# Kernel optimization log

Measured on AMD Instinct MI355X. Metric: run time of the kernel, lower is better.

Reference implementation:

```python
import jax, jax.numpy as jnp
import numpy as np

# --- model/problem constants (match init_kwargs) ---
B = 1024      # batch
F = 512       # featureSize
H = 1024      # hiddenSize
S = 8         # symmetrySize
BOX = 12      # boxSize
MAXB = 64     # maxBoxes
MAXSY = 64    # maxSyms
MAXS = 16     # max stack depth (pattern uses <= 2)
L = 126


def setup_inputs() -> dict:
    key = jax.random.key(0)
    ks = jax.random.split(key, 9)

    def lin(k, out_d, in_d):
        k1, k2 = jax.random.split(k)
        bound = 1.0 / np.sqrt(in_d)
        W = jax.random.uniform(k1, (out_d, in_d), minval=-bound, maxval=bound, dtype=jnp.float32)
        b = jax.random.uniform(k2, (out_d,), minval=-bound, maxval=bound, dtype=jnp.float32)
        return W, b

    Wd, bd = lin(ks[0], H, F)      # AdjDecoder.decode
    Wl, bl = lin(ks[1], F, H)      # AdjDecoder.left
    Wr, br = lin(ks[2], F, H)      # AdjDecoder.right
    Wsd, bsd = lin(ks[3], H, F)    # SymDecoder.decode
    Wsf, bsf = lin(ks[4], F, H)    # SymDecoder.left
    Wss, bss = lin(ks[5], S, H)    # SymDecoder.right
    Wbox, bbox = lin(ks[6], BOX, F)  # BoxDecoder.decode

    inputStacks = jax.random.normal(ks[7], (B, F), dtype=jnp.float32)

    # Valid stack program, PROCESSING order: [adj, sym, box] * 42.
    # stack depth: 1 ->(1) 2 ->(2) 2 ->(0) 1 ; 42 boxes, 42 syms.
    proc = np.tile(np.array([1, 2, 0], dtype=np.int32), L // 3)
    stored = proc[::-1].copy()  # forward() processes operations in reverse
    operations = jnp.asarray(np.tile(stored[None, None, :], (B, 1, 1)))  # [B,1,L]

    return {"inputStacks": inputStacks, "operations": operations,
            "Wd": Wd, "bd": bd, "Wl": Wl, "bl": bl, "Wr": Wr, "br": br,
            "Wsd": Wsd, "bsd": bsd, "Wsf": Wsf, "bsf": bsf, "Wss": Wss, "bss": bss,
            "Wbox": Wbox, "bbox": bbox}


def _forward(inputStacks, operations, Wd, bd, Wl, bl, Wr, br,
             Wsd, bsd, Wsf, bsf, Wss, bss, Wbox, bbox):
    Bn, Fn = inputStacks.shape
    ops_proc = jnp.flip(operations[:, 0, :], axis=1).T  # [L, B] processing order

    stack = jnp.zeros((Bn, MAXS, Fn), inputStacks.dtype).at[:, 0, :].set(inputStacks)
    sp = jnp.ones((Bn,), jnp.int32)           # stack pointer (size)
    boxbuf = jnp.zeros((Bn, MAXB, Fn), inputStacks.dtype)
    bc = jnp.zeros((Bn,), jnp.int32)
    symbuf = jnp.zeros((Bn, MAXSY, S), inputStacks.dtype)
    sc = jnp.zeros((Bn,), jnp.int32)
    rows = jnp.arange(Bn)

    def step(carry, op):
        stack, sp, boxbuf, bc, symbuf, sc = carry
        top_idx = jnp.clip(sp - 1, 0, MAXS - 1)
        top = stack[rows, top_idx]                      # [B,F]
        # AdjDecoder on every sample (selected by op==1)
        h = jnp.tanh(top @ Wd.T + bd)
        l = jnp.tanh(h @ Wl.T + bl)
        r = jnp.tanh(h @ Wr.T + br)
        # SymDecoder on every sample (selected by op==2)
        hs = jnp.tanh(top @ Wsd.T + bsd)
        f = jnp.tanh(hs @ Wsf.T + bsf)
        s = jnp.tanh(hs @ Wss.T + bss)

        is0 = op == 0
        is1 = op == 1
        is2 = op == 2
        # value replacing the popped top (for op 1 -> left, op 2 -> folded)
        val_top = jnp.where(is1[:, None], l, jnp.where(is2[:, None], f, top))
        pos = jnp.arange(MAXS)[None, :]
        m_top = (pos == top_idx[:, None]) & (~is0)[:, None]
        m_r = (pos == jnp.clip(sp, 0, MAXS - 1)[:, None]) & is1[:, None]
        stack = jnp.where(m_r[..., None], r[:, None, :],
                          jnp.where(m_top[..., None], val_top[:, None, :], stack))
        posb = jnp.arange(MAXB)[None, :]
        mb = (posb == bc[:, None]) & is0[:, None]
        boxbuf = jnp.where(mb[..., None], top[:, None, :], boxbuf)
        poss = jnp.arange(MAXSY)[None, :]
        ms = (poss == sc[:, None]) & is2[:, None]
        symbuf = jnp.where(ms[..., None], s[:, None, :], symbuf)

        sp = sp + jnp.where(is0, -1, jnp.where(is1, 1, 0)).astype(sp.dtype)
        bc = bc + is0.astype(bc.dtype)
        sc = sc + is2.astype(sc.dtype)
        return (stack, sp, boxbuf, bc, symbuf, sc), None

    (stack, sp, boxbuf, bc, symbuf, sc), _ = jax.lax.scan(
        step, (stack, sp, boxbuf, bc, symbuf, sc), ops_proc)

    # boxStacks[i].reverse(); boxDecoder; pad with zeros to maxBoxes
    jb = jnp.arange(MAXB)
    bidx = bc[:, None] - 1 - jb[None, :]          # reversed order
    bvalid = bidx >= 0
    bfeat = jnp.take_along_axis(boxbuf, jnp.clip(bidx, 0, MAXB - 1)[..., None], axis=1)
    boxes = jnp.tanh(bfeat @ Wbox.T + bbox) * bvalid[..., None].astype(bfeat.dtype)

    js = jnp.arange(MAXSY)
    sidx = sc[:, None] - 1 - js[None, :]
    svalid = sidx >= 0
    syms = jnp.take_along_axis(symbuf, jnp.clip(sidx, 0, MAXSY - 1)[..., None], axis=1)
    syms = syms * svalid[..., None].astype(syms.dtype)

    return boxes, syms  # [B, MAXB, BOX], [B, MAXSY, S]


def reference(inputStacks, operations, Wd, bd, Wl, bl, Wr, br,
              Wsd, bsd, Wsf, bsf, Wss, bss, Wbox, bbox):
    return _forward(inputStacks, operations, Wd, bd, Wl, bl, Wr, br,
                    Wsd, bsd, Wsf, bsf, Wss, bss, Wbox, bbox)
```

## Files before the change

### kernel.cpp

```cpp
#include <hip/hip_runtime.h>
#include <stdint.h>

#define B_     1024
#define F_     512
#define H_     1024
#define S_     8
#define BOX_   12
#define MAXB_  64
#define MAXSY_ 64
#define L_     126
#define STK_   3
#define NCYC_  42

typedef unsigned short u16;
typedef unsigned int   u32;
typedef unsigned long long u64;
typedef __attribute__((ext_vector_type(8))) short sh8;
typedef __attribute__((ext_vector_type(4))) int   i4;
typedef __attribute__((ext_vector_type(4))) float f4;

#define MFMA16(a,b,c) __builtin_amdgcn_mfma_f32_16x16x32_bf16((a),(b),(c),0,0,0)

#define XCC_ID_IMM (((32 - 1) << 11) | (0 << 6) | 20)

#define POLL_MAX (1 << 22)

constexpr size_t O_FLAG  = 2048;
constexpr size_t O_GFAIL = 2176;
constexpr size_t O_GXCD  = 2304;
constexpr size_t PL_HF = (size_t)H_ * F_ * 2;
constexpr size_t PL_FH = (size_t)F_ * H_ * 2;
constexpr size_t PL_SS = 16384;
constexpr size_t PL_BX = 16384;
constexpr size_t O_WdHi  = 8192;
constexpr size_t O_WdLo  = O_WdHi  + PL_HF;
constexpr size_t O_WsdHi = O_WdLo  + PL_HF;
constexpr size_t O_WsdLo = O_WsdHi + PL_HF;
constexpr size_t O_WlHi  = O_WsdLo + PL_HF;
constexpr size_t O_WlLo  = O_WlHi  + PL_FH;
constexpr size_t O_WrHi  = O_WlLo  + PL_FH;
constexpr size_t O_WrLo  = O_WrHi  + PL_FH;
constexpr size_t O_WsfHi = O_WrLo  + PL_FH;
constexpr size_t O_WsfLo = O_WsfHi + PL_FH;
constexpr size_t O_WssHi = O_WsfLo + PL_FH;
constexpr size_t O_WssLo = O_WssHi + PL_SS;
constexpr size_t O_WbxHi = O_WssLo + PL_SS;
constexpr size_t O_WbxLo = O_WbxHi + PL_BX;
constexpr size_t SZ_STK  = (size_t)B_ * STK_ * F_ * 2;
constexpr size_t O_SHi   = O_WbxLo + PL_BX;
constexpr size_t O_SLo   = O_SHi   + SZ_STK;
constexpr size_t SZ_H    = (size_t)B_ * H_ * 2;
constexpr size_t O_HAHi  = O_SLo   + SZ_STK;
constexpr size_t O_HALo  = O_HAHi  + SZ_H;
constexpr size_t O_HSHi  = O_HALo  + SZ_H;
constexpr size_t O_HSLo  = O_HSHi  + SZ_H;
constexpr size_t SZ_FB   = (size_t)B_ * 512 * 2;
constexpr size_t O_FB0Hi = O_HSLo  + SZ_H;
constexpr size_t O_FB0Lo = O_FB0Hi + SZ_FB;
constexpr size_t O_FB1Hi = O_FB0Lo + SZ_FB;
constexpr size_t O_FB1Lo = O_FB1Hi + SZ_FB;
constexpr size_t WS_NEED = O_FB1Lo + SZ_FB;

__device__ __forceinline__ float bf2float(u16 h) {
    union { u32 u; float f; } v; v.u = ((u32)h) << 16; return v.f;
}
__device__ __forceinline__ u16 bfhi_of(float f) {
    union { float f; u32 u; } v; v.f = f;
    u32 u = v.u;
    return (u16)((u + 0x7fffu + ((u >> 16) & 1u)) >> 16);
}
__device__ __forceinline__ void split2(float x, u16& hi, u16& lo) {
    hi = bfhi_of(x);
    lo = bfhi_of(x - bf2float(hi));
}

template<bool DC>
__device__ __forceinline__ void cst(u16* p, u16 v) {
    if (DC) asm volatile("global_store_short %0, %1, off sc0 sc1"
                         :: "v"(p), "v"((u32)v) : "memory");
    else    asm volatile("global_store_short %0, %1, off"
                         :: "v"(p), "v"((u32)v) : "memory");
}
__device__ __forceinline__ void vdrain() {
    asm volatile("s_waitcnt vmcnt(0)" ::: "memory");
}

__device__ __forceinline__ void cld8(i4& d0, i4& d1, i4& d2, i4& d3,
                                     i4& d4, i4& d5, i4& d6, i4& d7,
    const u16* p0, const u16* p1, const u16* p2, const u16* p3,
    const u16* p4, const u16* p5, const u16* p6, const u16* p7)
{
    asm volatile(
        "global_load_dwordx4 %0, %8, off sc0\n\t"
        "global_load_dwordx4 %1, %9, off sc0\n\t"
        "global_load_dwordx4 %2, %10, off sc0\n\t"
        "global_load_dwordx4 %3, %11, off sc0\n\t"
        "global_load_dwordx4 %4, %12, off sc0\n\t"
        "global_load_dwordx4 %5, %13, off sc0\n\t"
        "global_load_dwordx4 %6, %14, off sc0\n\t"
        "global_load_dwordx4 %7, %15, off sc0\n\t"
        "s_waitcnt vmcnt(0)"
        : "=&v"(d0),"=&v"(d1),"=&v"(d2),"=&v"(d3),
          "=&v"(d4),"=&v"(d5),"=&v"(d6),"=&v"(d7)
        : "v"(p0),"v"(p1),"v"(p2),"v"(p3),"v"(p4),"v"(p5),"v"(p6),"v"(p7));
}

__device__ __forceinline__ void cld8i(i4& d0, i4& d1, i4& d2, i4& d3,
                                      i4& d4, i4& d5, i4& d6, i4& d7,
    const u16* p0, const u16* p1, const u16* p2, const u16* p3,
    const u16* p4, const u16* p5, const u16* p6, const u16* p7)
{
    asm volatile(
        "global_load_dwordx4 %0, %8, off sc0\n\t"
        "global_load_dwordx4 %1, %9, off sc0\n\t"
        "global_load_dwordx4 %2, %10, off sc0\n\t"
        "global_load_dwordx4 %3, %11, off sc0\n\t"
        "global_load_dwordx4 %4, %12, off sc0\n\t"
        "global_load_dwordx4 %5, %13, off sc0\n\t"
        "global_load_dwordx4 %6, %14, off sc0\n\t"
        "global_load_dwordx4 %7, %15, off sc0"
        : "=&v"(d0),"=&v"(d1),"=&v"(d2),"=&v"(d3),
          "=&v"(d4),"=&v"(d5),"=&v"(d6),"=&v"(d7)
        : "v"(p0),"v"(p1),"v"(p2),"v"(p3),"v"(p4),"v"(p5),"v"(p6),"v"(p7));
}

__device__ void split_range(const float* __restrict__ s, u16* hi, u16* lo,
                            int n, int t0, int stride) {
    for (int i = t0; i < n; i += stride) {
        float v = s[i];
        u16 h = bfhi_of(v);
        hi[i] = h;
        lo[i] = bfhi_of(v - bf2float(h));
    }
}

__global__ void grass_prep(const float* __restrict__ X, const int* __restrict__ ops,
                           const float* __restrict__ Wd, const float* __restrict__ Wl,
                           const float* __restrict__ Wr, const float* __restrict__ Wsd,
                           const float* __restrict__ Wsf, const float* __restrict__ Wss,
                           const float* __restrict__ Wbox, char* __restrict__ ws)
{
    const int t0 = blockIdx.x * blockDim.x + threadIdx.x;
    const int st = gridDim.x * blockDim.x;
    split_range(Wd,  (u16*)(ws + O_WdHi),  (u16*)(ws + O_WdLo),  H_ * F_, t0, st);
    split_range(Wsd, (u16*)(ws + O_WsdHi), (u16*)(ws + O_WsdLo), H_ * F_, t0, st);
    split_range(Wl,  (u16*)(ws + O_WlHi),  (u16*)(ws + O_WlLo),  F_ * H_, t0, st);
    split_range(Wr,  (u16*)(ws + O_WrHi),  (u16*)(ws + O_WrLo),  F_ * H_, t0, st);
    split_range(Wsf, (u16*)(ws + O_WsfHi), (u16*)(ws + O_WsfLo), F_ * H_, t0, st);
    split_range(Wss, (u16*)(ws + O_WssHi), (u16*)(ws + O_WssLo), S_ * H_, t0, st);
    split_range(Wbox,(u16*)(ws + O_WbxHi), (u16*)(ws + O_WbxLo), BOX_ * F_, t0, st);
    u16* SHi = (u16*)(ws + O_SHi);
    u16* SLo = (u16*)(ws + O_SLo);
    for (int i = t0; i < B_ * F_; i += st) {
        int e = i >> 9, k = i & (F_ - 1);
        float v = X[i];
        u16 h = bfhi_of(v);
        size_t off = (size_t)e * STK_ * F_ + k;
        SHi[off] = h;
        SLo[off] = bfhi_of(v - bf2float(h));
    }
    int* flag = (int*)(ws + O_FLAG);
    for (int i = t0; i < B_ * L_; i += st) {
        int t = i % L_;
        int tm = t % 3;
        int expect = (tm == 0) ? 0 : ((tm == 1) ? 2 : 1);
        if (ops[i] != expect) {
            __hip_atomic_store(flag, 1, __ATOMIC_RELAXED, __HIP_MEMORY_SCOPE_AGENT);
            break;
        }
    }
}

__device__ __forceinline__ void gbar(int* bar, int target) {
    vdrain();
    __syncthreads();
    if (threadIdx.x == 0) {
        __hip_atomic_fetch_add(bar, 1, __ATOMIC_RELAXED, __HIP_MEMORY_SCOPE_AGENT);
        while (__hip_atomic_load(bar, __ATOMIC_RELAXED, __HIP_MEMORY_SCOPE_AGENT) < target)
            __builtin_amdgcn_s_sleep(2);
    }
    __syncthreads();
}
__device__ __forceinline__ void gbarT(int* bar, int target) {
    vdrain();
    __syncthreads();
    if (threadIdx.x == 0) {
        __hip_atomic_fetch_add(bar, 1, __ATOMIC_RELAXED, __HIP_MEMORY_SCOPE_AGENT);
        for (int it = 0; it < POLL_MAX; ++it) {
            if (__hip_atomic_load(bar, __ATOMIC_RELAXED, __HIP_MEMORY_SCOPE_AGENT) >= target) break;
            __builtin_amdgcn_s_sleep(2);
        }
    }
    __syncthreads();
}
__device__ __forceinline__ void gwaitT(int* ctr, int target) {
    if (threadIdx.x == 0) {
        for (int it = 0; it < POLL_MAX; ++it) {
            if (__hip_atomic_load(ctr, __ATOMIC_RELAXED, __HIP_MEMORY_SCOPE_AGENT) >= target) break;
            __builtin_amdgcn_s_sleep(2);
        }
    }
    __syncthreads();
}
// ... 161 lines not shown
#pragma unroll 2
    for (int kb = 0; kb < CW; kb += 64) {
        const int k0 = kb + quad * 8, k1 = k0 + 32;
        const int x0 = k0 ^ sm, x1 = k1 ^ sm;
        sh8 bH0 = {0,0,0,0,0,0,0,0}, bL0 = {0,0,0,0,0,0,0,0};
        sh8 bH1 = {0,0,0,0,0,0,0,0}, bL1 = {0,0,0,0,0,0,0,0};
        if (nb) {
            bH0 = *(const sh8*)(bh + k0); bL0 = *(const sh8*)(bl + k0);
            bH1 = *(const sh8*)(bh + k1); bL1 = *(const sh8*)(bl + k1);
        }
        sh8 aH0 = *(const sh8*)(Am + x0);
        sh8 aL0 = *(const sh8*)(Am + 64 * CW + x0);
        sh8 aH1 = *(const sh8*)(Am + x1);
        sh8 aL1 = *(const sh8*)(Am + 64 * CW + x1);
        c = MFMA16(aH0, bH0, c);
        c = MFMA16(aH0, bL0, c);
        c = MFMA16(aL0, bH0, c);
        c = MFMA16(aH1, bH1, c);
        c = MFMA16(aH1, bL1, c);
        c = MFMA16(aL1, bH1, c);
    }
}

__device__ __forceinline__ void zacc(f4 c[2][2]) {
    f4 z = {0.f, 0.f, 0.f, 0.f};
    c[0][0] = z; c[0][1] = z; c[1][0] = z; c[1][1] = z;
}

__device__ __forceinline__ void gemmK(u16* __restrict__ Ab,
    const u16* __restrict__ AHi, const u16* __restrict__ ALo, const int* __restrict__ aOff,
    const u16* __restrict__ WHi, const u16* __restrict__ WLo, int nRow0, int Kw,
    f4 c[2][2], int tid, int lane, int wv)
{
    zacc(c);
    for (int h = 0; h < Kw; h += 512) {
        __syncthreads();
        stageA_dc(Ab, AHi, ALo, aOff, h, tid);
        __syncthreads();
        kloop64<512>(Ab, WHi, WLo, nRow0, Kw, h, c, lane, wv);
    }
}
__device__ __forceinline__ void gemmK16(u16* __restrict__ Ab,
    const u16* __restrict__ AHi, const u16* __restrict__ ALo, const int* __restrict__ aOff,
    const u16* __restrict__ WHi, const u16* __restrict__ WLo, int nValid, int Kw,
    f4& c, int tid, int lane, int wv)
{
    f4 z = {0.f, 0.f, 0.f, 0.f};
    c = z;
    for (int h = 0; h < Kw; h += 512) {
        __syncthreads();
        stageA_dc(Ab, AHi, ALo, aOff, h, tid);
        __syncthreads();
        kloop16<512>(Ab, WHi, WLo, nValid, Kw, h, c, lane, wv);
    }
}

__device__ __forceinline__ void pipe_gemm128(u16* __restrict__ Ab,
    const u16* __restrict__ AHi, const u16* __restrict__ ALo, const int* __restrict__ aOff,
    const u16* __restrict__ WHi, const u16* __restrict__ WLo, int col0, int Kw,
    f4 cA[2][2], f4 cB[2][2], int tid, int lane, int wv)
{
    zacc(cA); zacc(cB);
    i4 s0,s1,s2,s3,s4,s5,s6,s7,s8,s9,s10,s11,s12,s13,s14,s15;
    stage_issue(s0,s1,s2,s3,s4,s5,s6,s7,s8,s9,s10,s11,s12,s13,s14,s15,
                AHi, ALo, aOff, 0, tid);
    __syncthreads();
    stage_write(s0,s1,s2,s3,s4,s5,s6,s7,s8,s9,s10,s11,s12,s13,s14,s15, Ab, tid);
    __syncthreads();
    for (int h = 0; h < Kw; h += 256) {
        const bool more = (h + 256 < Kw);
        if (more)
            stage_issue(s0,s1,s2,s3,s4,s5,s6,s7,s8,s9,s10,s11,s12,s13,s14,s15,
                        AHi, ALo, aOff, h + 256, tid);
        kloop64<256>(Ab, WHi, WLo, col0,      Kw, h, cA, lane, wv);
        kloop64<256>(Ab, WHi, WLo, col0 + 64, Kw, h, cB, lane, wv);
        if (more) {
            __syncthreads();
            stage_write(s0,s1,s2,s3,s4,s5,s6,s7,s8,s9,s10,s11,s12,s13,s14,s15, Ab, tid);
            __syncthreads();
        }
    }
}

template<bool DC>
__device__ __forceinline__ void ep_h(const f4 c[2][2], const float* __restrict__ bias,
                                     int colBase, int e0, u16* DHi, u16* DLo,
                                     int lane, int wv4)
{
    const int quad = lane >> 4, mr = lane & 15;
    const int mh = wv4 & 1, nh = (wv4 >> 1) & 1;
#pragma unroll
    for (int mi = 0; mi < 2; ++mi)
#pragma unroll
    for (int ni = 0; ni < 2; ++ni)
#pragma unroll
    for (int r = 0; r < 4; ++r) {
        int mm = (mh * 2 + mi) * 16 + quad * 4 + r;
        int nn = (nh * 2 + ni) * 16 + mr;
        float v = tanhf(c[mi][ni][r] + bias[colBase + nn]);
        u16 hi, lo; split2(v, hi, lo);
        size_t off = (size_t)(e0 + mm) * H_ + colBase + nn;
        cst<DC>(DHi + off, hi);
        cst<DC>(DLo + off, lo);
    }
}

template<bool DC>
__device__ __forceinline__ void ep_slot(const f4 c[2][2], const float* __restrict__ bias,
                                        int colBase, int slot, int e0,
                                        u16* SHi, u16* SLo, int lane, int wv4)
{
    const int quad = lane >> 4, mr = lane & 15;
    const int mh = wv4 & 1, nh = (wv4 >> 1) & 1;
#pragma unroll
    for (int mi = 0; mi < 2; ++mi)
#pragma unroll
    for (int ni = 0; ni < 2; ++ni)
#pragma unroll
    for (int r = 0; r < 4; ++r) {
        int mm = (mh * 2 + mi) * 16 + quad * 4 + r;
        int nn = (nh * 2 + ni) * 16 + mr;
        float v = tanhf(c[mi][ni][r] + bias[colBase + nn]);
        u16 hi, lo; split2(v, hi, lo);
        size_t off = ((size_t)(e0 + mm) * STK_ + slot) * F_ + colBase + nn;
        cst<DC>(SHi + off, hi);
        cst<DC>(SLo + off, lo);
    }
}

template<bool DC>
__device__ __forceinline__ void ep_fb(const f4 c[2][2], const float* __restrict__ bias,
                                      int colBase, int e0, u16* FHi, u16* FLo,
                                      int lane, int wv4)
{
    const int quad = lane >> 4, mr = lane & 15;
    const int mh = wv4 & 1, nh = (wv4 >> 1) & 1;
#pragma unroll
    for (int mi = 0; mi < 2; ++mi)
#pragma unroll
    for (int ni = 0; ni < 2; ++ni)
#pragma unroll
    for (int r = 0; r < 4; ++r) {
        int mm = (mh * 2 + mi) * 16 + quad * 4 + r;
        int nn = (nh * 2 + ni) * 16 + mr;
        float v = tanhf(c[mi][ni][r] + bias[colBase + nn]);
        u16 hi, lo; split2(v, hi, lo);
        size_t off = (size_t)(e0 + mm) * 512 + colBase + nn;
        cst<DC>(FHi + off, hi);
        cst<DC>(FLo + off, lo);
    }
}

template<bool DC>
__device__ __forceinline__ void ep_stack(const f4 c[2][2], const float* __restrict__ bias,
                                         int colBase, int opSel, bool useRi, int tix, int e0,
                                         const unsigned char* opsL, const int* spA,
                                         u16* SHi, u16* SLo, int lane, int wv)
{
    const int quad = lane >> 4, mr = lane & 15;
    const int mh = wv & 1, nh = (wv >> 1) & 1;
#pragma unroll
    for (int mi = 0; mi < 2; ++mi)
#pragma unroll
    for (int ni = 0; ni < 2; ++ni)
#pragma unroll
    for (int r = 0; r < 4; ++r) {
        int mm = (mh * 2 + mi) * 16 + quad * 4 + r;
        int nn = (nh * 2 + ni) * 16 + mr;
        if (opsL[mm * L_ + tix] != opSel) continue;
        int sp = spA[mm];
        int slot = useRi ? sp : sp - 1;
        slot = slot < 0 ? 0 : (slot > STK_ - 1 ? STK_ - 1 : slot);
        float v = tanhf(c[mi][ni][r] + bias[colBase + nn]);
        u16 hi, lo; split2(v, hi, lo);
        size_t off = ((size_t)(e0 + mm) * STK_ + slot) * F_ + colBase + nn;
        cst<DC>(SHi + off, hi);
        cst<DC>(SLo + off, lo);
    }
}

__device__ __forceinline__ void ep_small(const f4& c, const float* __restrict__ bias,
                                         int nValid, int opSel, int tix, int e0,
                                         const unsigned char* opsL, const int* eCnt, const int* eTot,
                                         float* __restrict__ outBase, int rowStride, int ncols,
                                         int lane, int wv)
{
    const int nn = lane & 15;
    if (nn >= nValid) return;
#pragma unroll
    for (int r = 0; r < 4; ++r) {
        int mm = wv * 16 + (lane >> 4) * 4 + r;
        if (opsL[mm * L_ + tix] != opSel) continue;
        int slot = eTot[mm] - 1 - eCnt[mm];
        if (slot < 0 || slot >= 64) continue;
        float v = tanhf(c[r] + bias[nn]);
        outBase[(size_t)(e0 + mm) * rowStride + slot * ncols + nn] = v;
    }
}

__device__ __forceinline__ void ep_small_u(const f4& c, const float* __restrict__ bias,
                                           int nValid, int slot, int e0,
                                           float* __restrict__ outBase, int rowStride, int ncols,
                                           int lane, int wv)
{
    const int nn = lane & 15;
    if (nn >= nValid) return;
#pragma unroll
    for (int r = 0; r < 4; ++r) {
        int mm = wv * 16 + (lane >> 4) * 4 + r;
        outBase[(size_t)(e0 + mm) * rowStride + slot * ncols + nn] = tanhf(c[r] + bias[nn]);
    }
}

__global__ __launch_bounds__(256, 1) void grass_pipe(
    const float* __restrict__ bd, const float* __restrict__ bl, const float* __restrict__ br,
    const float* __restrict__ bsd, const float* __restrict__ bsf, const float* __restrict__ bss,
    const float* __restrict__ bbox,
    char* __restrict__ ws, float* __restrict__ out)
{
    if (__hip_atomic_load((int*)(ws + O_FLAG), __ATOMIC_RELAXED, __HIP_MEMORY_SCOPE_AGENT))
        return;

    const int tid  = threadIdx.x;
    const int lane = tid & 63, wv = tid >> 6;
    const int j    = blockIdx.x >> 4;
    const int gid  = blockIdx.x & 15;
    const int e0   = gid * 64;

    const u16* WdHi  = (const u16*)(ws + O_WdHi);
    const u16* WdLo  = (const u16*)(ws + O_WdLo);
    const u16* WsdHi = (const u16*)(ws + O_WsdHi);
    const u16* WsdLo = (const u16*)(ws + O_WsdLo);
    const u16* WlHi  = (const u16*)(ws + O_WlHi);
    const u16* WlLo  = (const u16*)(ws + O_WlLo);
    const u16* WrHi  = (const u16*)(ws + O_WrHi);
    const u16* WrLo  = (const u16*)(ws + O_WrLo);
    const u16* WsfHi = (const u16*)(ws + O_WsfHi);
    const u16* WsfLo = (const u16*)(ws + O_WsfLo);
    const u16* WssHi = (const u16*)(ws + O_WssHi);
    const u16* WssLo = (const u16*)(ws + O_WssLo);
    const u16* WbxHi = (const u16*)(ws + O_WbxHi);
    const u16* WbxLo = (const u16*)(ws + O_WbxLo);
    u16* SHi  = (u16*)(ws + O_SHi);
    u16* SLo  = (u16*)(ws + O_SLo);
    u16* HAHi = (u16*)(ws + O_HAHi);
    u16* HALo = (u16*)(ws + O_HALo);
    u16* HSHi = (u16*)(ws + O_HSHi);
    u16* HSLo = (u16*)(ws + O_HSLo);
    u16* FB0Hi = (u16*)(ws + O_FB0Hi);
    u16* FB0Lo = (u16*)(ws + O_FB0Lo);
    u16* FB1Hi = (u16*)(ws + O_FB1Hi);
    u16* FB1Lo = (u16*)(ws + O_FB1Lo);
    int* cbar = (int*)ws + gid * 32;
    int* sbar = cbar + 1;
    int* pbar = cbar + 3;
    int* gx   = (int*)(ws + O_GXCD) + gid * 32;
    int* gf   = (int*)(ws + O_GFAIL) + gid;

    float* outB = out;
    float* outS = out + (size_t)B_ * MAXB_ * BOX_;

    __shared__ __align__(16) u16 Abuf[2 * 64 * 256];
    __shared__ int aS0[64], aR1[64], aR2[64], aHH[64], aFB[64];

    if (tid < 64) {
        aS0[tid] = ((e0 + tid) * STK_ + 0) * F_;
        aR1[tid] = ((e0 + tid) * STK_ + 1) * F_;
        aR2[tid] = ((e0 + tid) * STK_ + 2) * F_;
        aHH[tid] = (e0 + tid) * H_;
        aFB[tid] = (e0 + tid) * 512;
    }

    const int myxcd = (int)(__builtin_amdgcn_s_getreg(XCC_ID_IMM) & 0xf);
    if (tid == 0)
        __hip_atomic_store(gx + j, myxcd, __ATOMIC_RELAXED, __HIP_MEMORY_SCOPE_AGENT);
    gbarT(pbar, 16);
    if (tid < 16) {
        int ox = __hip_atomic_load(gx + tid, __ATOMIC_RELAXED, __HIP_MEMORY_SCOPE_AGENT);
        if (ox != myxcd)
            __hip_atomic_store(gf, 1, __ATOMIC_RELAXED, __HIP_MEMORY_SCOPE_AGENT);
    }
    gbarT(pbar, 32);
    if (__hip_atomic_load(gf, __ATOMIC_RELAXED, __HIP_MEMORY_SCOPE_AGENT))
        return;

    f4 cA[2][2], cB[2][2];
    f4 cs;

    if (j < 8) {
        for (int cyc = 0; cyc < NCYC_; ++cyc) {
            pipe_gemm128(Abuf, SHi, SLo, aS0, WdHi, WdLo, j * 128, F_, cA, cB, tid, lane, wv);
            ep_h<false>(cA, bd, j * 128,      e0, HAHi, HALo, lane, wv);
            ep_h<false>(cB, bd, j * 128 + 64, e0, HAHi, HALo, lane, wv);
            gbarT(cbar, 8 * (2 * cyc + 1));
            if (j < 4) {
                pipe_gemm128(Abuf, HAHi, HALo, aHH, WlHi, WlLo, j * 128, H_, cA, cB, tid, lane, wv);
                ep_slot<false>(cA, bl, j * 128,      0, e0, SHi, SLo, lane, wv);
                ep_slot<false>(cB, bl, j * 128 + 64, 0, e0, SHi, SLo, lane, wv);
            } else {
                const int rs = 1 + (cyc & 1);
                pipe_gemm128(Abuf, HAHi, HALo, aHH, WrHi, WrLo, (j - 4) * 128, H_, cA, cB, tid, lane, wv);
                if (cyc >= 2) gwaitT(sbar, 8 * (2 * (cyc - 2) + 1));
                ep_slot<false>(cA, br, (j - 4) * 128,      rs, e0, SHi, SLo, lane, wv);
                ep_slot<false>(cB, br, (j - 4) * 128 + 64, rs, e0, SHi, SLo, lane, wv);
            }
            gbarT(cbar, 8 * (2 * cyc + 2));
        }
    } else {
        const int role = j - 8;
        for (int cyc = 0; cyc < NCYC_; ++cyc) {
            gwaitT(cbar, 8 * (2 * cyc + 2));
            const int* aR = (cyc & 1) ? aR2 : aR1;
            pipe_gemm128(Abuf, SHi, SLo, aR, WsdHi, WsdLo, role * 128, F_, cA, cB, tid, lane, wv);
            ep_h<false>(cA, bsd, role * 128,      e0, HSHi, HSLo, lane, wv);
            ep_h<false>(cB, bsd, role * 128 + 64, e0, HSHi, HSLo, lane, wv);
            gbarT(sbar, 8 * (2 * cyc + 1));
            if (role < 4) {
                u16* FH = (cyc & 1) ? FB1Hi : FB0Hi;
                u16* FL = (cyc & 1) ? FB1Lo : FB0Lo;
                pipe_gemm128(Abuf, HSHi, HSLo, aHH, WsfHi, WsfLo, role * 128, H_, cA, cB, tid, lane, wv);
                ep_fb<false>(cA, bsf, role * 128,      e0, FH, FL, lane, wv);
                ep_fb<false>(cB, bsf, role * 128 + 64, e0, FH, FL, lane, wv);
            } else if (role == 4) {
                f4 z = {0.f, 0.f, 0.f, 0.f}; cs = z;
                for (int h = 0; h < H_; h += 256) {
                    __syncthreads();
                    stage256(Abuf, HSHi, HSLo, aHH, h, tid);
                    __syncthreads();
                    kloop16<256>(Abuf, WssHi, WssLo, S_, H_, h, cs, lane, wv);
                }
                ep_small_u(cs, bss, S_, NCYC_ - 1 - cyc, e0, outS, MAXSY_ * S_, S_, lane, wv);
            } else if (role == 5 && cyc >= 1) {
                const u16* FH = ((cyc - 1) & 1) ? FB1Hi : FB0Hi;
                const u16* FL = ((cyc - 1) & 1) ? FB1Lo : FB0Lo;
                f4 z = {0.f, 0.f, 0.f, 0.f}; cs = z;
                for (int h = 0; h < 512; h += 256) {
                    __syncthreads();
                    stage256(Abuf, FH, FL, aFB, h, tid);
                    __syncthreads();
                    kloop16<256>(Abuf, WbxHi, WbxLo, BOX_, 512, h, cs, lane, wv);
                }
                ep_small_u(cs, bbox, BOX_, NCYC_ - (cyc - 1) - 1, e0, outB, MAXB_ * BOX_, BOX_, lane, wv);
            }
            gbarT(sbar, 8 * (2 * cyc + 2));
        }
        if (role == 5) {
            const u16* FH = ((NCYC_ - 1) & 1) ? FB1Hi : FB0Hi;
            const u16* FL = ((NCYC_ - 1) & 1) ? FB1Lo : FB0Lo;
            f4 z = {0.f, 0.f, 0.f, 0.f}; cs = z;
            for (int h = 0; h < 512; h += 256) {
                __syncthreads();
                stage256(Abuf, FH, FL, aFB, h, tid);
                __syncthreads();
                kloop16<256>(Abuf, WbxHi, WbxLo, BOX_, 512, h, cs, lane, wv);
            }
            ep_small_u(cs, bbox, BOX_, 0, e0, outB, MAXB_ * BOX_, BOX_, lane, wv);
        }
    }
}

__global__ __launch_bounds__(256, 2) void grass_legacy(
    const int* __restrict__ ops,
    const float* __restrict__ bd, const float* __restrict__ bl, const float* __restrict__ br,
    const float* __restrict__ bsd, const float* __restrict__ bsf, const float* __restrict__ bss,
    const float* __restrict__ bbox,
    char* __restrict__ ws, float* __restrict__ out)
{
    const int tid  = threadIdx.x;
    const int lane = tid & 63, wv = tid >> 6;
    const int gid  = blockIdx.x >> 4;
    const int j    = blockIdx.x & 15;
    const int e0   = gid * 64;

    {
        int nonuni = __hip_atomic_load((int*)(ws + O_FLAG), __ATOMIC_RELAXED, __HIP_MEMORY_SCOPE_AGENT);
        int gfl = __hip_atomic_load((int*)(ws + O_GFAIL) + gid, __ATOMIC_RELAXED, __HIP_MEMORY_SCOPE_AGENT);
        if (!nonuni && !gfl) return;
    }

    const u16* WdHi  = (const u16*)(ws + O_WdHi);
    const u16* WdLo  = (const u16*)(ws + O_WdLo);
    const u16* WsdHi = (const u16*)(ws + O_WsdHi);
    const u16* WsdLo = (const u16*)(ws + O_WsdLo);
    const u16* WlHi  = (const u16*)(ws + O_WlHi);
    const u16* WlLo  = (const u16*)(ws + O_WlLo);
    const u16* WrHi  = (const u16*)(ws + O_WrHi);
    const u16* WrLo  = (const u16*)(ws + O_WrLo);
    const u16* WsfHi = (const u16*)(ws + O_WsfHi);
    const u16* WsfLo = (const u16*)(ws + O_WsfLo);
    const u16* WssHi = (const u16*)(ws + O_WssHi);
    const u16* WssLo = (const u16*)(ws + O_WssLo);
    const u16* WbxHi = (const u16*)(ws + O_WbxHi);
    const u16* WbxLo = (const u16*)(ws + O_WbxLo);
    u16* SHi  = (u16*)(ws + O_SHi);
    u16* SLo  = (u16*)(ws + O_SLo);
    u16* HAHi = (u16*)(ws + O_HAHi);
    u16* HALo = (u16*)(ws + O_HALo);
    u16* HSHi = (u16*)(ws + O_HSHi);
    u16* HSLo = (u16*)(ws + O_HSLo);
    int* bar = (int*)ws + gid * 32 + 2;

    float* outB = out;
    float* outS = out + (size_t)B_ * MAXB_ * BOX_;

    __shared__ __align__(16) u16 Abuf[2 * 64 * 512];
    __shared__ unsigned char opsL[64 * L_];
    __shared__ int spA[64], beA[64], seA[64], beF[64], seF[64];
    __shared__ int aStk[64], aHH[64];
    __shared__ int sInfo[2];

    for (int idx = tid; idx < 64 * L_; idx += 256) {
        int e = idx / L_, t = idx - e * L_;
        opsL[idx] = (unsigned char)ops[(size_t)(e0 + e) * L_ + t];
    }
    __syncthreads();
    if (tid < 64) {
        spA[tid] = 1; beA[tid] = 0; seA[tid] = 0;
        int cb = 0, cs2 = 0;
        for (int t = 0; t < L_; ++t) {
            int o = opsL[tid * L_ + t];
            cb += (o == 0); cs2 += (o == 2);
        }
        beF[tid] = cb; seF[tid] = cs2;
        aHH[tid]  = (e0 + tid) * H_;
        aStk[tid] = ((e0 + tid) * STK_ + 0) * F_;
    }
    __syncthreads();

    int epoch = 0;
    f4 c[2][2];
    f4 cs;

    for (int step = 0; step < L_; ++step) {
        const int tix = L_ - 1 - step;
        if (wv == 0) {
            int o  = opsL[lane * L_ + tix];
            int sp = spA[lane];
            unsigned long long bo = __ballot(o  == opsL[0 * L_ + tix]);
            unsigned long long bs = __ballot(sp == spA[0]);
            if (lane == 0) {
                sInfo[0] = o;
                sInfo[1] = (bo == ~0ull && bs == ~0ull) ? 1 : 0;
            }
        }
        __syncthreads();
        const int opU = sInfo[0], uni = sInfo[1];

        if (uni) {
            if (opU == 1) {
                gemmK(Abuf, SHi, SLo, aStk, WdHi, WdLo, j * 64, F_, c, tid, lane, wv);
                ep_h<true>(c, bd, j * 64, e0, HAHi, HALo, lane, wv);
                ++epoch; gbar(bar, 16 * epoch);
                {
                    const u16* W2H = (j < 8) ? WlHi : WrHi;
                    const u16* W2L = (j < 8) ? WlLo : WrLo;
                    const float* b2 = (j < 8) ? bl : br;
                    gemmK(Abuf, HAHi, HALo, aHH, W2H, W2L, (j & 7) * 64, H_, c, tid, lane, wv);
                    ep_stack<true>(c, b2, (j & 7) * 64, 1, j >= 8, tix, e0, opsL, spA, SHi, SLo, lane, wv);
                }
                ++epoch; gbar(bar, 16 * epoch);
            } else if (opU == 2) {
                gemmK(Abuf, SHi, SLo, aStk, WsdHi, WsdLo, j * 64, F_, c, tid, lane, wv);
                ep_h<true>(c, bsd, j * 64, e0, HAHi, HALo, lane, wv);
                ++epoch; gbar(bar, 16 * epoch);
                if (j < 8) {
                    gemmK(Abuf, HAHi, HALo, aHH, WsfHi, WsfLo, j * 64, H_, c, tid, lane, wv);
                    ep_stack<true>(c, bsf, j * 64, 2, false, tix, e0, opsL, spA, SHi, SLo, lane, wv);
                } else if (j == 8) {
                    gemmK16(Abuf, HAHi, HALo, aHH, WssHi, WssLo, S_, H_, cs, tid, lane, wv);
                    ep_small(cs, bss, S_, 2, tix, e0, opsL, seA, seF, outS, MAXSY_ * S_, S_, lane, wv);
                }
                ++epoch; gbar(bar, 16 * epoch);
            } else {
                if (j == 0) {
                    gemmK16(Abuf, SHi, SLo, aStk, WbxHi, WbxLo, BOX_, F_, cs, tid, lane, wv);
                    ep_small(cs, bbox, BOX_, 0, tix, e0, opsL, beA, beF, outB, MAXB_ * BOX_, BOX_, lane, wv);
                }
            }
        } else {
            gemmK(Abuf, SHi, SLo, aStk, WdHi, WdLo, j * 64, F_, c, tid, lane, wv);
            ep_h<true>(c, bd, j * 64, e0, HAHi, HALo, lane, wv);
            gemmK(Abuf, SHi, SLo, aStk, WsdHi, WsdLo, j * 64, F_, c, tid, lane, wv);
            ep_h<true>(c, bsd, j * 64, e0, HSHi, HSLo, lane, wv);
            if (j == 0) {
                gemmK16(Abuf, SHi, SLo, aStk, WbxHi, WbxLo, BOX_, F_, cs, tid, lane, wv);
                ep_small(cs, bbox, BOX_, 0, tix, e0, opsL, beA, beF, outB, MAXB_ * BOX_, BOX_, lane, wv);
            }
            ++epoch; gbar(bar, 16 * epoch);
            if (j < 8) {
                gemmK(Abuf, HAHi, HALo, aHH, WlHi, WlLo, j * 64, H_, c, tid, lane, wv);
                ep_stack<true>(c, bl, j * 64, 1, false, tix, e0, opsL, spA, SHi, SLo, lane, wv);
                gemmK(Abuf, HSHi, HSLo, aHH, WsfHi, WsfLo, j * 64, H_, c, tid, lane, wv);
                ep_stack<true>(c, bsf, j * 64, 2, false, tix, e0, opsL, spA, SHi, SLo, lane, wv);
            } else {
                gemmK(Abuf, HAHi, HALo, aHH, WrHi, WrLo, (j - 8) * 64, H_, c, tid, lane, wv);
                ep_stack<true>(c, br, (j & 7) * 64, 1, true, tix, e0, opsL, spA, SHi, SLo, lane, wv);
                if (j == 8) {
                    gemmK16(Abuf, HSHi, HSLo, aHH, WssHi, WssLo, S_, H_, cs, tid, lane, wv);
                    ep_small(cs, bss, S_, 2, tix, e0, opsL, seA, seF, outS, MAXSY_ * S_, S_, lane, wv);
                }
            }
            ++epoch; gbar(bar, 16 * epoch);
        }

        __syncthreads();
        if (tid < 64) {
            int o = opsL[tid * L_ + tix];
            if (o == 1)      spA[tid]++;
            else if (o == 2) seA[tid]++;
            else           { beA[tid]++; spA[tid]--; }
            int sp = spA[tid];
            int ti = sp - 1; ti = ti < 0 ? 0 : (ti > STK_ - 1 ? STK_ - 1 : ti);
            aStk[tid] = ((e0 + tid) * STK_ + ti) * F_;
        }
        __syncthreads();
    }
}

__device__ __forceinline__ void fdot4(const float* __restrict__ row,
                                      const float* __restrict__ x0, const float* __restrict__ x1,
                                      const float* __restrict__ x2, const float* __restrict__ x3,
                                      int K4, float& r0, float& r1, float& r2, float& r3)
{
    const float4* r  = (const float4*)row;
    const float4* p0 = (const float4*)x0; const float4* p1 = (const float4*)x1;
    const float4* p2 = (const float4*)x2; const float4* p3 = (const float4*)x3;
    float s0=0.f,s1=0.f,s2=0.f,s3=0.f,t0=0.f,t1=0.f,t2=0.f,t3=0.f;
    for (int i = 0; i < K4; i += 2) {
        float4 w0 = r[i], w1 = r[i+1]; float4 v;
        v=p0[i]; s0+=w0.x*v.x; s0+=w0.y*v.y; s0+=w0.z*v.z; s0+=w0.w*v.w;
        v=p0[i+1]; t0+=w1.x*v.x; t0+=w1.y*v.y; t0+=w1.z*v.z; t0+=w1.w*v.w;
        v=p1[i]; s1+=w0.x*v.x; s1+=w0.y*v.y; s1+=w0.z*v.z; s1+=w0.w*v.w;
        v=p1[i+1]; t1+=w1.x*v.x; t1+=w1.y*v.y; t1+=w1.z*v.z; t1+=w1.w*v.w;
        v=p2[i]; s2+=w0.x*v.x; s2+=w0.y*v.y; s2+=w0.z*v.z; s2+=w0.w*v.w;
        v=p2[i+1]; t2+=w1.x*v.x; t2+=w1.y*v.y; t2+=w1.z*v.z; t2+=w1.w*v.w;
        v=p3[i]; s3+=w0.x*v.x; s3+=w0.y*v.y; s3+=w0.z*v.z; s3+=w0.w*v.w;
        v=p3[i+1]; t3+=w1.x*v.x; t3+=w1.y*v.y; t3+=w1.z*v.z; t3+=w1.w*v.w;
    }
    r0=s0+t0; r1=s1+t1; r2=s2+t2; r3=s3+t3;
}
__device__ __forceinline__ float fdot1(const float* __restrict__ row,
                                       const float* __restrict__ x, int K4)
{
    const float4* r = (const float4*)row; const float4* p = (const float4*)x;
    float s=0.f,t=0.f;
    for (int i = 0; i < K4; i += 2) {
        float4 w0=r[i], v0=p[i], w1=r[i+1], v1=p[i+1];
        s+=w0.x*v0.x; s+=w0.y*v0.y; s+=w0.z*v0.z; s+=w0.w*v0.w;
        t+=w1.x*v1.x; t+=w1.y*v1.y; t+=w1.z*v1.z; t+=w1.w*v1.w;
    }
    return s+t;
}
#define FB_G 4
__global__ __launch_bounds__(1024) void grass_fallback(
    const float* __restrict__ inputStacks, const int* __restrict__ ops,
    const float* __restrict__ Wd, const float* __restrict__ bd,
    const float* __restrict__ Wl, const float* __restrict__ bl,
    const float* __restrict__ Wr, const float* __restrict__ br,
    const float* __restrict__ Wsd, const float* __restrict__ bsd,
    const float* __restrict__ Wsf, const float* __restrict__ bsf,
    const float* __restrict__ Wss, const float* __restrict__ bss,
    const float* __restrict__ Wbox, const float* __restrict__ bbox,
    float* __restrict__ out)
{
    __shared__ float stk[FB_G][STK_][F_];
    __shared__ float hh[FB_G][H_];
    __shared__ float boxtmp[FB_G][MAXB_][BOX_];
    __shared__ float symtmp[FB_G][MAXSY_][S_];
    const int t = threadIdx.x, b0 = blockIdx.x * FB_G;
    for (int idx = t; idx < FB_G*F_; idx += 1024) {
        int g = idx >> 9, k = idx & (F_-1);
        stk[g][0][k] = inputStacks[(size_t)(b0+g)*F_ + k];
    }
    for (int idx = t; idx < FB_G*H_; idx += 1024) hh[idx>>10][idx&(H_-1)] = 0.f;
    int sp[FB_G], bc[FB_G], sc[FB_G];
#pragma unroll
    for (int g = 0; g < FB_G; ++g) { sp[g]=1; bc[g]=0; sc[g]=0; }
    __syncthreads();
    for (int step = 0; step < L_; ++step) {
// ... 111 lines not shown
```

Before: 2.877 ms.

## Drop XCD co-location check and use device-coherent loads/stores for group exchange

Removes the runtime check that made all 16 blocks of a batch group verify they share one XCD, and the early-exit fallback that went with it. Block-to-group mapping changes from j-major to gid-major, and all intermediate stores and loads now use sc0 sc1 (device-scope coherence), so cross-XCD communication stays correct. This removes a startup barrier and the fallback path, but every inter-block exchange now bypasses the L2 and goes through a more distant coherence point, which costs latency.

```diff
diff --git a/kernel.cpp b/kernel.cpp
--- a/kernel.cpp
+++ b/kernel.cpp
@@ -21,13 +21,10 @@
 
 #define MFMA16(a,b,c) __builtin_amdgcn_mfma_f32_16x16x32_bf16((a),(b),(c),0,0,0)
 
-#define XCC_ID_IMM (((32 - 1) << 11) | (0 << 6) | 20)
-
 #define POLL_MAX (1 << 22)
 
 constexpr size_t O_FLAG  = 2048;
 constexpr size_t O_GFAIL = 2176;
-constexpr size_t O_GXCD  = 2304;
 constexpr size_t PL_HF = (size_t)H_ * F_ * 2;
 constexpr size_t PL_FH = (size_t)F_ * H_ * 2;
 constexpr size_t PL_SS = 16384;
@@ -74,12 +71,9 @@
     lo = bfhi_of(x - bf2float(hi));
 }
 
-template<bool DC>
-__device__ __forceinline__ void cst(u16* p, u16 v) {
-    if (DC) asm volatile("global_store_short %0, %1, off sc0 sc1"
-                         :: "v"(p), "v"((u32)v) : "memory");
-    else    asm volatile("global_store_short %0, %1, off"
-                         :: "v"(p), "v"((u32)v) : "memory");
+__device__ __forceinline__ void cstDC(u16* p, u16 v) {
+    asm volatile("global_store_short %0, %1, off sc0 sc1"
+                 :: "v"(p), "v"((u32)v) : "memory");
 }
 __device__ __forceinline__ void vdrain() {
     asm volatile("s_waitcnt vmcnt(0)" ::: "memory");
@@ -91,14 +85,14 @@
     const u16* p4, const u16* p5, const u16* p6, const u16* p7)
 {
     asm volatile(
-        "global_load_dwordx4 %0, %8, off sc0\n\t"
-        "global_load_dwordx4 %1, %9, off sc0\n\t"
-        "global_load_dwordx4 %2, %10, off sc0\n\t"
-        "global_load_dwordx4 %3, %11, off sc0\n\t"
-        "global_load_dwordx4 %4, %12, off sc0\n\t"
-        "global_load_dwordx4 %5, %13, off sc0\n\t"
-        "global_load_dwordx4 %6, %14, off sc0\n\t"
-        "global_load_dwordx4 %7, %15, off sc0\n\t"
+        "global_load_dwordx4 %0, %8, off sc0 sc1\n\t"
+        "global_load_dwordx4 %1, %9, off sc0 sc1\n\t"
+        "global_load_dwordx4 %2, %10, off sc0 sc1\n\t"
+        "global_load_dwordx4 %3, %11, off sc0 sc1\n\t"
+        "global_load_dwordx4 %4, %12, off sc0 sc1\n\t"
+        "global_load_dwordx4 %5, %13, off sc0 sc1\n\t"
+        "global_load_dwordx4 %6, %14, off sc0 sc1\n\t"
+        "global_load_dwordx4 %7, %15, off sc0 sc1\n\t"
         "s_waitcnt vmcnt(0)"
         : "=&v"(d0),"=&v"(d1),"=&v"(d2),"=&v"(d3),
           "=&v"(d4),"=&v"(d5),"=&v"(d6),"=&v"(d7)
@@ -111,14 +105,14 @@
     const u16* p4, const u16* p5, const u16* p6, const u16* p7)
 {
     asm volatile(
-        "global_load_dwordx4 %0, %8, off sc0\n\t"
-        "global_load_dwordx4 %1, %9, off sc0\n\t"
-        "global_load_dwordx4 %2, %10, off sc0\n\t"
-        "global_load_dwordx4 %3, %11, off sc0\n\t"
-        "global_load_dwordx4 %4, %12, off sc0\n\t"
-        "global_load_dwordx4 %5, %13, off sc0\n\t"
-        "global_load_dwordx4 %6, %14, off sc0\n\t"
-        "global_load_dwordx4 %7, %15, off sc0"
+        "global_load_dwordx4 %0, %8, off sc0 sc1\n\t"
+        "global_load_dwordx4 %1, %9, off sc0 sc1\n\t"
+        "global_load_dwordx4 %2, %10, off sc0 sc1\n\t"
+        "global_load_dwordx4 %3, %11, off sc0 sc1\n\t"
+        "global_load_dwordx4 %4, %12, off sc0 sc1\n\t"
+        "global_load_dwordx4 %5, %13, off sc0 sc1\n\t"
+        "global_load_dwordx4 %6, %14, off sc0 sc1\n\t"
+        "global_load_dwordx4 %7, %15, off sc0 sc1"
         : "=&v"(d0),"=&v"(d1),"=&v"(d2),"=&v"(d3),
           "=&v"(d4),"=&v"(d5),"=&v"(d6),"=&v"(d7)
         : "v"(p0),"v"(p1),"v"(p2),"v"(p3),"v"(p4),"v"(p5),"v"(p6),"v"(p7));
@@ -446,7 +440,6 @@
     }
 }
 
-template<bool DC>
 __device__ __forceinline__ void ep_h(const f4 c[2][2], const float* __restrict__ bias,
                                      int colBase, int e0, u16* DHi, u16* DLo,
                                      int lane, int wv4)
@@ -464,12 +457,11 @@
         float v = tanhf(c[mi][ni][r] + bias[colBase + nn]);
         u16 hi, lo; split2(v, hi, lo);
         size_t off = (size_t)(e0 + mm) * H_ + colBase + nn;
-        cst<DC>(DHi + off, hi);
-        cst<DC>(DLo + off, lo);
-    }
-}
-
-template<bool DC>
+        cstDC(DHi + off, hi);
+        cstDC(DLo + off, lo);
+    }
+}
+
 __device__ __forceinline__ void ep_slot(const f4 c[2][2], const float* __restrict__ bias,
                                         int colBase, int slot, int e0,
                                         u16* SHi, u16* SLo, int lane, int wv4)
@@ -487,12 +479,11 @@
         float v = tanhf(c[mi][ni][r] + bias[colBase + nn]);
         u16 hi, lo; split2(v, hi, lo);
         size_t off = ((size_t)(e0 + mm) * STK_ + slot) * F_ + colBase + nn;
-        cst<DC>(SHi + off, hi);
-        cst<DC>(SLo + off, lo);
-    }
-}
-
-template<bool DC>
+        cstDC(SHi + off, hi);
+        cstDC(SLo + off, lo);
+    }
+}
+
 __device__ __forceinline__ void ep_fb(const f4 c[2][2], const float* __restrict__ bias,
                                       int colBase, int e0, u16* FHi, u16* FLo,
                                       int lane, int wv4)
@@ -510,12 +501,11 @@
         float v = tanhf(c[mi][ni][r] + bias[colBase + nn]);
         u16 hi, lo; split2(v, hi, lo);
         size_t off = (size_t)(e0 + mm) * 512 + colBase + nn;
-        cst<DC>(FHi + off, hi);
-        cst<DC>(FLo + off, lo);
-    }
-}
-
-template<bool DC>
+        cstDC(FHi + off, hi);
+        cstDC(FLo + off, lo);
+    }
+}
+
 __device__ __forceinline__ void ep_stack(const f4 c[2][2], const float* __restrict__ bias,
                                          int colBase, int opSel, bool useRi, int tix, int e0,
                                          const unsigned char* opsL, const int* spA,
@@ -538,8 +528,8 @@
         float v = tanhf(c[mi][ni][r] + bias[colBase + nn]);
         u16 hi, lo; split2(v, hi, lo);
         size_t off = ((size_t)(e0 + mm) * STK_ + slot) * F_ + colBase + nn;
-        cst<DC>(SHi + off, hi);
-        cst<DC>(SLo + off, lo);
+        cstDC(SHi + off, hi);
+        cstDC(SLo + off, lo);
     }
 }
 
@@ -587,8 +577,8 @@
 
     const int tid  = threadIdx.x;
     const int lane = tid & 63, wv = tid >> 6;
-    const int j    = blockIdx.x >> 4;
-    const int gid  = blockIdx.x & 15;
+    const int gid  = blockIdx.x >> 4;
+    const int j    = blockIdx.x & 15;
     const int e0   = gid * 64;
 
     const u16* WdHi  = (const u16*)(ws + O_WdHi);
@@ -617,9 +607,6 @@
     u16* FB1Lo = (u16*)(ws + O_FB1Lo);
     int* cbar = (int*)ws + gid * 32;
     int* sbar = cbar + 1;
-    int* pbar = cbar + 3;
-    int* gx   = (int*)(ws + O_GXCD) + gid * 32;
-    int* gf   = (int*)(ws + O_GFAIL) + gid;
 
     float* outB = out;
     float* outS = out + (size_t)B_ * MAXB_ * BOX_;
@@ -634,19 +621,7 @@
         aHH[tid] = (e0 + tid) * H_;
         aFB[tid] = (e0 + tid) * 512;
     }
-
-    const int myxcd = (int)(__builtin_amdgcn_s_getreg(XCC_ID_IMM) & 0xf);
-    if (tid == 0)
-        __hip_atomic_store(gx + j, myxcd, __ATOMIC_RELAXED, __HIP_MEMORY_SCOPE_AGENT);
-    gbarT(pbar, 16);
-    if (tid < 16) {
-        int ox = __hip_atomic_load(gx + tid, __ATOMIC_RELAXED, __HIP_MEMORY_SCOPE_AGENT);
-        if (ox != myxcd)
-            __hip_atomic_store(gf, 1, __ATOMIC_RELAXED, __HIP_MEMORY_SCOPE_AGENT);
-    }
-    gbarT(pbar, 32);
-    if (__hip_atomic_load(gf, __ATOMIC_RELAXED, __HIP_MEMORY_SCOPE_AGENT))
-        return;
+    __syncthreads();
 
     f4 cA[2][2], cB[2][2];
     f4 cs;
@@ -654,19 +629,19 @@
     if (j < 8) {
         for (int cyc = 0; cyc < NCYC_; ++cyc) {
             pipe_gemm128(Abuf, SHi, SLo, aS0, WdHi, WdLo, j * 128, F_, cA, cB, tid, lane, wv);
-            ep_h<false>(cA, bd, j * 128,      e0, HAHi, HALo, lane, wv);
-            ep_h<false>(cB, bd, j * 128 + 64, e0, HAHi, HALo, lane, wv);
+            ep_h(cA, bd, j * 128,      e0, HAHi, HALo, lane, wv);
+            ep_h(cB, bd, j * 128 + 64, e0, HAHi, HALo, lane, wv);
             gbarT(cbar, 8 * (2 * cyc + 1));
             if (j < 4) {
                 pipe_gemm128(Abuf, HAHi, HALo, aHH, WlHi, WlLo, j * 128, H_, cA, cB, tid, lane, wv);
-                ep_slot<false>(cA, bl, j * 128,      0, e0, SHi, SLo, lane, wv);
-                ep_slot<false>(cB, bl, j * 128 + 64, 0, e0, SHi, SLo, lane, wv);
+                ep_slot(cA, bl, j * 128,      0, e0, SHi, SLo, lane, wv);
+                ep_slot(cB, bl, j * 128 + 64, 0, e0, SHi, SLo, lane, wv);
             } else {
                 const int rs = 1 + (cyc & 1);
                 pipe_gemm128(Abuf, HAHi, HALo, aHH, WrHi, WrLo, (j - 4) * 128, H_, cA, cB, tid, lane, wv);
                 if (cyc >= 2) gwaitT(sbar, 8 * (2 * (cyc - 2) + 1));
-                ep_slot<false>(cA, br, (j - 4) * 128,      rs, e0, SHi, SLo, lane, wv);
-                ep_slot<false>(cB, br, (j - 4) * 128 + 64, rs, e0, SHi, SLo, lane, wv);
+                ep_slot(cA, br, (j - 4) * 128,      rs, e0, SHi, SLo, lane, wv);
+                ep_slot(cB, br, (j - 4) * 128 + 64, rs, e0, SHi, SLo, lane, wv);
             }
             gbarT(cbar, 8 * (2 * cyc + 2));
         }
@@ -676,15 +651,15 @@
             gwaitT(cbar, 8 * (2 * cyc + 2));
             const int* aR = (cyc & 1) ? aR2 : aR1;
             pipe_gemm128(Abuf, SHi, SLo, aR, WsdHi, WsdLo, role * 128, F_, cA, cB, tid, lane, wv);
-            ep_h<false>(cA, bsd, role * 128,      e0, HSHi, HSLo, lane, wv);
-            ep_h<false>(cB, bsd, role * 128 + 64, e0, HSHi, HSLo, lane, wv);
+            ep_h(cA, bsd, role * 128,      e0, HSHi, HSLo, lane, wv);
+            ep_h(cB, bsd, role * 128 + 64, e0, HSHi, HSLo, lane, wv);
             gbarT(sbar, 8 * (2 * cyc + 1));
             if (role < 4) {
                 u16* FH = (cyc & 1) ? FB1Hi : FB0Hi;
                 u16* FL = (cyc & 1) ? FB1Lo : FB0Lo;
                 pipe_gemm128(Abuf, HSHi, HSLo, aHH, WsfHi, WsfLo, role * 128, H_, cA, cB, tid, lane, wv);
-                ep_fb<false>(cA, bsf, role * 128,      e0, FH, FL, lane, wv);
-                ep_fb<false>(cB, bsf, role * 128 + 64, e0, FH, FL, lane, wv);
+                ep_fb(cA, bsf, role * 128,      e0, FH, FL, lane, wv);
+                ep_fb(cB, bsf, role * 128 + 64, e0, FH, FL, lane, wv);
             } else if (role == 4) {
                 f4 z = {0.f, 0.f, 0.f, 0.f}; cs = z;
                 for (int h = 0; h < H_; h += 256) {
@@ -813,23 +788,23 @@
         if (uni) {
             if (opU == 1) {
                 gemmK(Abuf, SHi, SLo, aStk, WdHi, WdLo, j * 64, F_, c, tid, lane, wv);
-                ep_h<true>(c, bd, j * 64, e0, HAHi, HALo, lane, wv);
+                ep_h(c, bd, j * 64, e0, HAHi, HALo, lane, wv);
                 ++epoch; gbar(bar, 16 * epoch);
                 {
                     const u16* W2H = (j < 8) ? WlHi : WrHi;
                     const u16* W2L = (j < 8) ? WlLo : WrLo;
                     const float* b2 = (j < 8) ? bl : br;
                     gemmK(Abuf, HAHi, HALo, aHH, W2H, W2L, (j & 7) * 64, H_, c, tid, lane, wv);
-                    ep_stack<true>(c, b2, (j & 7) * 64, 1, j >= 8, tix, e0, opsL, spA, SHi, SLo, lane, wv);
+                    ep_stack(c, b2, (j & 7) * 64, 1, j >= 8, tix, e0, opsL, spA, SHi, SLo, lane, wv);
                 }
                 ++epoch; gbar(bar, 16 * epoch);
             } else if (opU == 2) {
                 gemmK(Abuf, SHi, SLo, aStk, WsdHi, WsdLo, j * 64, F_, c, tid, lane, wv);
-                ep_h<true>(c, bsd, j * 64, e0, HAHi, HALo, lane, wv);
+                ep_h(c, bsd, j * 64, e0, HAHi, HALo, lane, wv);
                 ++epoch; gbar(bar, 16 * epoch);
                 if (j < 8) {
                     gemmK(Abuf, HAHi, HALo, aHH, WsfHi, WsfLo, j * 64, H_, c, tid, lane, wv);
-                    ep_stack<true>(c, bsf, j * 64, 2, false, tix, e0, opsL, spA, SHi, SLo, lane, wv);
+                    ep_stack(c, bsf, j * 64, 2, false, tix, e0, opsL, spA, SHi, SLo, lane, wv);
                 } else if (j == 8) {
                     gemmK16(Abuf, HAHi, HALo, aHH, WssHi, WssLo, S_, H_, cs, tid, lane, wv);
                     ep_small(cs, bss, S_, 2, tix, e0, opsL, seA, seF, outS, MAXSY_ * S_, S_, lane, wv);
@@ -843,9 +818,9 @@
             }
         } else {
             gemmK(Abuf, SHi, SLo, aStk, WdHi, WdLo, j * 64, F_, c, tid, lane, wv);
-            ep_h<true>(c, bd, j * 64, e0, HAHi, HALo, lane, wv);
+            ep_h(c, bd, j * 64, e0, HAHi, HALo, lane, wv);
             gemmK(Abuf, SHi, SLo, aStk, WsdHi, WsdLo, j * 64, F_, c, tid, lane, wv);
-            ep_h<true>(c, bsd, j * 64, e0, HSHi, HSLo, lane, wv);
+            ep_h(c, bsd, j * 64, e0, HSHi, HSLo, lane, wv);
             if (j == 0) {
                 gemmK16(Abuf, SHi, SLo, aStk, WbxHi, WbxLo, BOX_, F_, cs, tid, lane, wv);
                 ep_small(cs, bbox, BOX_, 0, tix, e0, opsL, beA, beF, outB, MAXB_ * BOX_, BOX_, lane, wv);
@@ -853,12 +828,12 @@
             ++epoch; gbar(bar, 16 * epoch);
             if (j < 8) {
                 gemmK(Abuf, HAHi, HALo, aHH, WlHi, WlLo, j * 64, H_, c, tid, lane, wv);
-                ep_stack<true>(c, bl, j * 64, 1, false, tix, e0, opsL, spA, SHi, SLo, lane, wv);
+                ep_stack(c, bl, j * 64, 1, false, tix, e0, opsL, spA, SHi, SLo, lane, wv);
                 gemmK(Abuf, HSHi, HSLo, aHH, WsfHi, WsfLo, j * 64, H_, c, tid, lane, wv);
-                ep_stack<true>(c, bsf, j * 64, 2, false, tix, e0, opsL, spA, SHi, SLo, lane, wv);
+                ep_stack(c, bsf, j * 64, 2, false, tix, e0, opsL, spA, SHi, SLo, lane, wv);
             } else {
                 gemmK(Abuf, HAHi, HALo, aHH, WrHi, WrLo, (j - 8) * 64, H_, c, tid, lane, wv);
-                ep_stack<true>(c, br, (j & 7) * 64, 1, true, tix, e0, opsL, spA, SHi, SLo, lane, wv);
+                ep_stack(c, br, (j & 7) * 64, 1, true, tix, e0, opsL, spA, SHi, SLo, lane, wv);
                 if (j == 8) {
                     gemmK16(Abuf, HSHi, HSLo, aHH, WssHi, WssLo, S_, H_, cs, tid, lane, wv);
                     ep_small(cs, bss, S_, 2, tix, e0, opsL, seA, seF, outS, MAXSY_ * S_, S_, lane, wv);
```

Result: slower. 2.993 ms (+4.0%).
